# Performance work log

Hardware: AMD Instinct MI355X
Metric: run time of the kernel (lower is better)

## Reference

```python
import jax, jax.numpy as jnp
import numpy as np

EMBED = 1024
HEADS = 16
HEAD_DIM = EMBED // HEADS
BASE = 10000.0


def _rope_cos_sin(seq_len, dim, dtype):
    inv_freq = 1.0 / (BASE ** (jnp.arange(0, dim, 2, dtype=jnp.float32) / dim))
    t = jnp.arange(seq_len, dtype=jnp.float32)
    freqs = jnp.einsum('i,j->ij', t, inv_freq)           # [S, dim/2]
    emb = jnp.concatenate([freqs, freqs], axis=-1)        # [S, dim]
    return jnp.cos(emb).astype(dtype), jnp.sin(emb).astype(dtype)


def _rotate_half(x):
    d = x.shape[-1] // 2
    return jnp.concatenate([-x[..., d:], x[..., :d]], axis=-1)


def setup_inputs() -> dict:
    key = jax.random.key(0)
    ks = jax.random.split(key, 7)
    B, S = 2, 2048
    scale = 0.02
    return {
        'query': jax.random.normal(ks[0], (B, S, EMBED), jnp.float32),
        'key': jax.random.normal(ks[1], (B, S, EMBED), jnp.float32),
        'value': jax.random.normal(ks[2], (B, S, EMBED), jnp.float32),
        'Wq': jax.random.normal(ks[3], (EMBED, EMBED), jnp.float32) * scale,
        'Wk': jax.random.normal(ks[4], (EMBED, EMBED), jnp.float32) * scale,
        'Wv': jax.random.normal(ks[5], (EMBED, EMBED), jnp.float32) * scale,
        'Wo': jax.random.normal(ks[6], (EMBED, EMBED), jnp.float32) * scale,
    }


def reference(query, key, value, Wq, Wk, Wv, Wo):
    B, Sq, _ = query.shape
    Sk = key.shape[1]
    # projections (bias-free Linear: x @ W^T; W sampled so use x @ W directly)
    q = (query @ Wq).reshape(B, Sq, HEADS, HEAD_DIM).transpose(0, 2, 1, 3)  # [B,H,Sq,Dh]
    k = (key @ Wk).reshape(B, Sk, HEADS, HEAD_DIM).transpose(0, 2, 1, 3)
    v = (value @ Wv).reshape(B, Sk, HEADS, HEAD_DIM).transpose(0, 2, 1, 3)
    # RoPE applied to q and k per-position
    cos_q, sin_q = _rope_cos_sin(Sq, HEAD_DIM, q.dtype)  # [Sq,Dh]
    cos_k, sin_k = _rope_cos_sin(Sk, HEAD_DIM, k.dtype)
    q = q * cos_q[None, None] + _rotate_half(q) * sin_q[None, None]
    k = k * cos_k[None, None] + _rotate_half(k) * sin_k[None, None]
    scores = jnp.einsum('bhqd,bhkd->bhqk', q, k) / jnp.sqrt(jnp.asarray(HEAD_DIM, q.dtype))
    probs = jax.nn.softmax(scores, axis=-1)
    out = jnp.einsum('bhqk,bhkd->bhqd', probs, v)
    out = out.transpose(0, 2, 1, 3).reshape(B, Sq, EMBED)
    return out @ Wo
```

## Files before the change

### kernel.cpp

```cpp
#include <hip/hip_runtime.h>
#include <hip/hip_bf16.h>


typedef unsigned short u16;
typedef unsigned int u32;
typedef __attribute__((ext_vector_type(8))) short short8;
typedef __attribute__((ext_vector_type(4))) float f32x4;

#define MFMA16(a, b, c) __builtin_amdgcn_mfma_f32_16x16x32_bf16((a), (b), (c), 0, 0, 0)

typedef __attribute__((address_space(3))) u16 lds_u16;
typedef __attribute__((address_space(1))) const u16 glb_u16;

__device__ __forceinline__ void gload16(const u16* g, u16* l) {
    __builtin_amdgcn_global_load_lds((glb_u16*)g, (lds_u16*)l, 16, 0, 0);
}

__device__ __forceinline__ u16 f2bf(float f) {
    __hip_bfloat16 h = __float2bfloat16(f);
    return *reinterpret_cast<u16*>(&h);
}

__global__ __launch_bounds__(256) void conv_x(const float* __restrict__ q,
                                              const float* __restrict__ k,
                                              const float* __restrict__ v,
                                              u16* __restrict__ X3) {
    int z = blockIdx.y;
    const float* src = (z == 0) ? q : (z == 1) ? k : v;
    int i = (blockIdx.x * 256 + threadIdx.x) * 4;
    float4 f = *reinterpret_cast<const float4*>(src + i);
    ushort4 o;
    o.x = f2bf(f.x); o.y = f2bf(f.y); o.z = f2bf(f.z); o.w = f2bf(f.w);
    *reinterpret_cast<ushort4*>(X3 + (size_t)z * 4194304 + i) = o;
}

__global__ __launch_bounds__(256) void transpose_w(const float* __restrict__ w0,
                                                   const float* __restrict__ w1,
                                                   const float* __restrict__ w2,
                                                   const float* __restrict__ w3,
                                                   u16* __restrict__ WT) {
    __shared__ float t[32][33];
    const float* Ws[4] = {w0, w1, w2, w3};
    const float* W = Ws[blockIdx.z];
    int n0 = blockIdx.x * 32, k0 = blockIdx.y * 32;
    int tx = threadIdx.x, ty = threadIdx.y;
    for (int r = 0; r < 4; r++) {
        int kk = ty + r * 8;
        t[kk][tx] = W[(k0 + kk) * 1024 + n0 + tx];
    }
    __syncthreads();
    u16* out = WT + (size_t)blockIdx.z * 1048576;
    for (int r = 0; r < 4; r++) {
        int nn = ty + r * 8;
        out[(n0 + nn) * 1024 + k0 + tx] = f2bf(t[tx][nn]);
    }
}

__global__ __launch_bounds__(256) void rope_table(float2* __restrict__ tab) {
    int gid = blockIdx.x * 256 + threadIdx.x;
    int s = gid >> 5, d = gid & 31;
    float inv = powf(10000.f, -(float)d / 32.f);
    float fr = (float)s * inv;
    tab[gid] = make_float2(cosf(fr), sinf(fr));
}

__global__ __launch_bounds__(256) void gemm_qkv(const u16* __restrict__ Aall,
                                                const u16* __restrict__ WT,
                                                u16* __restrict__ Qp,
                                                u16* __restrict__ Kp,
                                                u16* __restrict__ Vsd,
                                                const float2* __restrict__ tab) {
    int z = blockIdx.z;
    const u16* A  = Aall + (size_t)z * 4194304;
    const u16* Bt = WT + (size_t)z * 1048576;
    const int K = 1024;
    int m0 = blockIdx.y * 128, n0 = blockIdx.x * 128;
    __shared__ u16 As[128 * 32];
    __shared__ u16 Bs[128 * 32];
    int tid = threadIdx.x;
    int wave = tid >> 6, lane = tid & 63, quad = lane >> 4, l16 = lane & 15;
    int wm = (wave >> 1) * 64, wn = (wave & 1) * 64;
    f32x4 acc[4][4];
    for (int i = 0; i < 4; i++)
        for (int j = 0; j < 4; j++)
            for (int r = 0; r < 4; r++) acc[i][j][r] = 0.f;

    for (int k0 = 0; k0 < K; k0 += 32) {
        __syncthreads();
        for (int c = 0; c < 2; c++) {
            int e = (tid + c * 256) * 8;
            int row = e >> 5, col = e & 31;
            gload16(&A[(size_t)(m0 + row) * K + k0 + col], &As[e]);
            gload16(&Bt[(size_t)(n0 + row) * K + k0 + col], &Bs[e]);
        }
        __syncthreads();
        short8 af[4], bfr[4];
        for (int i = 0; i < 4; i++)
            af[i] = *reinterpret_cast<const short8*>(&As[(wm + i * 16 + l16) * 32 + quad * 8]);
        for (int j = 0; j < 4; j++)
            bfr[j] = *reinterpret_cast<const short8*>(&Bs[(wn + j * 16 + l16) * 32 + quad * 8]);
        for (int i = 0; i < 4; i++)
            for (int j = 0; j < 4; j++)
                acc[i][j] = MFMA16(af[i], bfr[j], acc[i][j]);
    }

    int h = (n0 + wn) >> 6;
    if (z == 2) {
        for (int i = 0; i < 4; i++)
            for (int r = 0; r < 4; r++) {
                int m = m0 + wm + i * 16 + quad * 4 + r;
                int b = m >> 11, s = m & 2047;
                u16* row = Vsd + (((size_t)(b * 16 + h)) * 2048 + s) * 64;
                for (int j = 0; j < 4; j++)
                    row[j * 16 + l16] = f2bf(acc[i][j][r]);
            }
    } else {
        u16* base = (z == 0) ? Qp : Kp;
        float scale = (z == 0) ? 0.125f : 1.f;
        for (int i = 0; i < 4; i++)
            for (int r = 0; r < 4; r++) {
                int m = m0 + wm + i * 16 + quad * 4 + r;
                int b = m >> 11, s = m & 2047;
                u16* row = base + (((size_t)(b * 16 + h)) * 2048 + s) * 64;
                for (int j = 0; j < 2; j++) {
                    int d = j * 16 + l16;
                    float2 cs = tab[s * 32 + d];
                    float x1 = acc[i][j][r] * scale;
                    float x2 = acc[i][j + 2][r] * scale;
                    row[d]      = f2bf(x1 * cs.x - x2 * cs.y);
                    row[d + 32] = f2bf(x2 * cs.x + x1 * cs.y);
                }
            }
    }
}

__global__ __launch_bounds__(256) void gemm_bt_f32(const u16* __restrict__ A,
                                                   const u16* __restrict__ Bt,
                                                   float* __restrict__ C,
                                                   int M, int N, int K) {
    int m0 = blockIdx.y * 128, n0 = blockIdx.x * 128;
    __shared__ u16 As[128 * 32];
    __shared__ u16 Bs[128 * 32];
    int tid = threadIdx.x;
    int wave = tid >> 6, lane = tid & 63, quad = lane >> 4, l16 = lane & 15;
    int wm = (wave >> 1) * 64, wn = (wave & 1) * 64;
    f32x4 acc[4][4];
    for (int i = 0; i < 4; i++)
        for (int j = 0; j < 4; j++)
            for (int r = 0; r < 4; r++) acc[i][j][r] = 0.f;

    for (int k0 = 0; k0 < K; k0 += 32) {
        __syncthreads();
        for (int c = 0; c < 2; c++) {
            int e = (tid + c * 256) * 8;
            int row = e >> 5, col = e & 31;
            gload16(&A[(size_t)(m0 + row) * K + k0 + col], &As[e]);
            gload16(&Bt[(size_t)(n0 + row) * K + k0 + col], &Bs[e]);
        }
        __syncthreads();
        short8 af[4], bfr[4];
        for (int i = 0; i < 4; i++)
            af[i] = *reinterpret_cast<const short8*>(&As[(wm + i * 16 + l16) * 32 + quad * 8]);
        for (int j = 0; j < 4; j++)
            bfr[j] = *reinterpret_cast<const short8*>(&Bs[(wn + j * 16 + l16) * 32 + quad * 8]);
        for (int i = 0; i < 4; i++)
            for (int j = 0; j < 4; j++)
                acc[i][j] = MFMA16(af[i], bfr[j], acc[i][j]);
    }

    for (int i = 0; i < 4; i++)
        for (int r = 0; r < 4; r++) {
            int m = m0 + wm + i * 16 + quad * 4 + r;
            for (int j = 0; j < 4; j++)
                C[(size_t)m * N + n0 + wn + j * 16 + l16] = acc[i][j][r];
        }
}

__global__ __launch_bounds__(256) void v_transpose(const u16* __restrict__ Vsd,
                                                   u16* __restrict__ Vt) {
    __shared__ u16 t[64 * 72];
    int s0 = blockIdx.x * 64, bh = blockIdx.y;
    const u16* src = Vsd + (size_t)bh * 131072;
    int tid = threadIdx.x;
    int srow = tid >> 3, scol = (tid & 7) * 8;
    for (int c = 0; c < 2; c++) {
        int s = srow + c * 32;
        *reinterpret_cast<int4*>(&t[s * 72 + scol]) =
            *reinterpret_cast<const int4*>(&src[(size_t)(s0 + s) * 64 + scol]);
    }
    __syncthreads();
    for (int c = 0; c < 2; c++) {
        int d = srow + c * 32;
        short8 o;
        for (int j = 0; j < 8; j++) o[j] = (short)t[(scol + j) * 72 + d];
        *reinterpret_cast<short8*>(&Vt[(size_t)bh * 131072 + (size_t)d * 2048 + s0 + scol]) = o;
    }
}

__global__ __launch_bounds__(256) void flash_attn(const u16* __restrict__ Qp,
                                                  const u16* __restrict__ Kp,
                                                  const u16* __restrict__ Vt_g,
                                                  u16* __restrict__ attn) {
    int q0 = blockIdx.x * 128, bh = blockIdx.y;
    const u16* Q = Qp + (size_t)bh * 131072;
    const u16* K = Kp + (size_t)bh * 131072;
    const u16* Vt = Vt_g + (size_t)bh * 131072;
    __shared__ u16 Ks[64 * 72];
    __shared__ u16 Vs[64 * 72];
    __shared__ u16 Ps[128 * 72];
    int tid = threadIdx.x, wave = tid >> 6, lane = tid & 63;
    int quad = lane >> 4, l16 = lane & 15;
    int srow = tid >> 3, scol = (tid & 7) * 8;

    short8 qf[2][2];
    for (int g = 0; g < 2; g++)
        for (int kk = 0; kk < 2; kk++)
            qf[g][kk] = *reinterpret_cast<const short8*>(
                &Q[(size_t)(q0 + wave * 32 + g * 16 + l16) * 64 + kk * 32 + quad * 8]);

    float psum[2] = {0.f, 0.f};
    f32x4 Oacc[2][4];
    for (int g = 0; g < 2; g++)
        for (int dt = 0; dt < 4; dt++)
            for (int r = 0; r < 4; r++) Oacc[g][dt][r] = 0.f;

    for (int kv0 = 0; kv0 < 2048; kv0 += 64) {
        __syncthreads();
        for (int c = 0; c < 2; c++) {
            int row = srow + c * 32;
            *reinterpret_cast<int4*>(&Ks[row * 72 + scol]) =
                *reinterpret_cast<const int4*>(&K[(size_t)(kv0 + row) * 64 + scol]);
            *reinterpret_cast<int4*>(&Vs[row * 72 + scol]) =
                *reinterpret_cast<const int4*>(&Vt[(size_t)row * 2048 + kv0 + scol]);
        }
        __syncthreads();

        f32x4 st[2][4];
        for (int g = 0; g < 2; g++)
            for (int nt = 0; nt < 4; nt++)
                for (int r = 0; r < 4; r++) st[g][nt][r] = 0.f;
        for (int kk = 0; kk < 2; kk++)
            for (int nt = 0; nt < 4; nt++) {
                short8 af = *reinterpret_cast<const short8*>(
                    &Ks[(nt * 16 + l16) * 72 + kk * 32 + quad * 8]);
                for (int g = 0; g < 2; g++)
                    st[g][nt] = MFMA16(af, qf[g][kk], st[g][nt]);
            }

        for (int g = 0; g < 2; g++)
            for (int nt = 0; nt < 4; nt++) {
                float p0 = __expf(st[g][nt][0]);
                float p1 = __expf(st[g][nt][1]);
                float p2 = __expf(st[g][nt][2]);
                float p3 = __expf(st[g][nt][3]);
                psum[g] += (p0 + p1) + (p2 + p3);
                uint2 w;
                w.x = (u32)f2bf(p0) | ((u32)f2bf(p1) << 16);
                w.y = (u32)f2bf(p2) | ((u32)f2bf(p3) << 16);
                *reinterpret_cast<uint2*>(
                    &Ps[(wave * 32 + g * 16 + l16) * 72 + nt * 16 + quad * 4]) = w;
            }

        for (int kk = 0; kk < 2; kk++) {
            short8 pa[2];
            for (int g = 0; g < 2; g++)
                pa[g] = *reinterpret_cast<const short8*>(
                    &Ps[(wave * 32 + g * 16 + l16) * 72 + kk * 32 + quad * 8]);
            for (int dt = 0; dt < 4; dt++) {
                short8 bv = *reinterpret_cast<const short8*>(
                    &Vs[(dt * 16 + l16) * 72 + kk * 32 + quad * 8]);
                for (int g = 0; g < 2; g++)
                    Oacc[g][dt] = MFMA16(pa[g], bv, Oacc[g][dt]);
            }
        }
    }

    int b = bh >> 4, h = bh & 15;
    for (int g = 0; g < 2; g++) {
        float ps = psum[g];
        ps += __shfl_xor(ps, 16);
        ps += __shfl_xor(ps, 32);
        float linv[4];
        for (int r = 0; r < 4; r++)
            linv[r] = 1.f / __shfl(ps, quad * 4 + r);
        for (int dt = 0; dt < 4; dt++)
            for (int r = 0; r < 4; r++) {
                int s = q0 + wave * 32 + g * 16 + quad * 4 + r;
                attn[((size_t)(b * 2048 + s)) * 1024 + h * 64 + dt * 16 + l16] =
                    f2bf(Oacc[g][dt][r] * linv[r]);
            }
    }
}

extern "C" void kernel_launch(void* const* d_in, const int* in_sizes, int n_in,
                              void* d_out, int out_size, void* d_ws, size_t ws_size,
                              hipStream_t stream) {
    const float* q  = (const float*)d_in[0];
    const float* k  = (const float*)d_in[1];
    const float* v  = (const float*)d_in[2];
    const float* wq = (const float*)d_in[3];
    const float* wk = (const float*)d_in[4];
    const float* wv = (const float*)d_in[5];
    const float* wo = (const float*)d_in[6];

    u16* ws = (u16*)d_ws;
    u16* WT  = ws;
    u16* X3  = ws + (size_t)4 * 1048576;
    u16* QKV = X3 + (size_t)3 * 4194304;
    u16* Qp  = QKV;
    u16* Kp  = QKV + (size_t)1 * 4194304;
    u16* Vsd = QKV + (size_t)2 * 4194304;
    u16* attn = X3;
    u16* Vt_g = X3 + (size_t)2 * 4194304;
    float2* tab = (float2*)d_out;

    conv_x<<<dim3(4096, 3), 256, 0, stream>>>(q, k, v, X3);
    transpose_w<<<dim3(32, 32, 4), dim3(32, 8), 0, stream>>>(wq, wk, wv, wo, WT);
    rope_table<<<256, 256, 0, stream>>>(tab);
    gemm_qkv<<<dim3(8, 32, 3), 256, 0, stream>>>(X3, WT, Qp, Kp, Vsd, tab);
    v_transpose<<<dim3(32, 32), 256, 0, stream>>>(Vsd, Vt_g);
    flash_attn<<<dim3(16, 32), 256, 0, stream>>>(Qp, Kp, Vt_g, attn);
    gemm_bt_f32<<<dim3(8, 32, 1), 256, 0, stream>>>(
        attn, WT + (size_t)3 * 1048576, (float*)d_out, 4096, 1024, 1024);
}
```

Measured before the change: 275.9 us.

## Split KV tile across wave halves in flash attention with LDS reduction

Restructures the attention kernel to use 512 threads per block over 64 query rows. Each block loads a 128-key tile, and two groups of four waves each process one 64-key half. At the end the partial outputs and row sums are combined through shared memory. Blocks double from 512 to 1024, which is meant to fill more CUs and raise occupancy. In exchange the kernel pays for extra LDS traffic, a final cross-wave reduction with added syncs, and a larger per-block LDS footprint. The code skips max subtraction, which the original version also relied on.

```diff
diff --git a/kernel.cpp b/kernel.cpp
--- a/kernel.cpp
+++ b/kernel.cpp
@@ -197,97 +197,104 @@
     }
 }
 
-__global__ __launch_bounds__(256) void flash_attn(const u16* __restrict__ Qp,
-                                                  const u16* __restrict__ Kp,
-                                                  const u16* __restrict__ Vt_g,
-                                                  u16* __restrict__ attn) {
-    int q0 = blockIdx.x * 128, bh = blockIdx.y;
+__global__ __launch_bounds__(512, 6) void flash_attn(const u16* __restrict__ Qp,
+                                                     const u16* __restrict__ Kp,
+                                                     const u16* __restrict__ Vt_g,
+                                                     u16* __restrict__ attn) {
+    int q0 = blockIdx.x * 64, bh = blockIdx.y;
     const u16* Q = Qp + (size_t)bh * 131072;
     const u16* K = Kp + (size_t)bh * 131072;
     const u16* Vt = Vt_g + (size_t)bh * 131072;
-    __shared__ u16 Ks[64 * 72];
-    __shared__ u16 Vs[64 * 72];
-    __shared__ u16 Ps[128 * 72];
+    __shared__ u16 Ks[128 * 72];
+    __shared__ u16 Vs[64 * 136];
+    __shared__ u16 Ps[64 * 136];
     int tid = threadIdx.x, wave = tid >> 6, lane = tid & 63;
     int quad = lane >> 4, l16 = lane & 15;
-    int srow = tid >> 3, scol = (tid & 7) * 8;
-
-    short8 qf[2][2];
-    for (int g = 0; g < 2; g++)
-        for (int kk = 0; kk < 2; kk++)
-            qf[g][kk] = *reinterpret_cast<const short8*>(
-                &Q[(size_t)(q0 + wave * 32 + g * 16 + l16) * 64 + kk * 32 + quad * 8]);
-
-    float psum[2] = {0.f, 0.f};
-    f32x4 Oacc[2][4];
-    for (int g = 0; g < 2; g++)
-        for (int dt = 0; dt < 4; dt++)
-            for (int r = 0; r < 4; r++) Oacc[g][dt][r] = 0.f;
-
-    for (int kv0 = 0; kv0 < 2048; kv0 += 64) {
+    int qg = wave & 3;
+    int kh = wave >> 2;
+
+    short8 qf[2];
+    for (int kk = 0; kk < 2; kk++)
+        qf[kk] = *reinterpret_cast<const short8*>(
+            &Q[(size_t)(q0 + qg * 16 + l16) * 64 + kk * 32 + quad * 8]);
+
+    float psum = 0.f;
+    f32x4 Oacc[4];
+    for (int dt = 0; dt < 4; dt++)
+        for (int r = 0; r < 4; r++) Oacc[dt][r] = 0.f;
+
+    for (int kv0 = 0; kv0 < 2048; kv0 += 128) {
         __syncthreads();
         for (int c = 0; c < 2; c++) {
-            int row = srow + c * 32;
-            *reinterpret_cast<int4*>(&Ks[row * 72 + scol]) =
-                *reinterpret_cast<const int4*>(&K[(size_t)(kv0 + row) * 64 + scol]);
-            *reinterpret_cast<int4*>(&Vs[row * 72 + scol]) =
-                *reinterpret_cast<const int4*>(&Vt[(size_t)row * 2048 + kv0 + scol]);
-        }
-        __syncthreads();
-
-        f32x4 st[2][4];
-        for (int g = 0; g < 2; g++)
-            for (int nt = 0; nt < 4; nt++)
-                for (int r = 0; r < 4; r++) st[g][nt][r] = 0.f;
+            int idx = tid + c * 512;
+            int krow = idx >> 3, kcol = (idx & 7) * 8;
+            *reinterpret_cast<int4*>(&Ks[krow * 72 + kcol]) =
+                *reinterpret_cast<const int4*>(&K[(size_t)(kv0 + krow) * 64 + kcol]);
+            int vrow = idx >> 4, vcol = (idx & 15) * 8;
+            *reinterpret_cast<int4*>(&Vs[vrow * 136 + vcol]) =
+                *reinterpret_cast<const int4*>(&Vt[(size_t)vrow * 2048 + kv0 + vcol]);
+        }
+        __syncthreads();
+
+        f32x4 st[4];
+        for (int nt = 0; nt < 4; nt++)
+            for (int r = 0; r < 4; r++) st[nt][r] = 0.f;
         for (int kk = 0; kk < 2; kk++)
             for (int nt = 0; nt < 4; nt++) {
                 short8 af = *reinterpret_cast<const short8*>(
-                    &Ks[(nt * 16 + l16) * 72 + kk * 32 + quad * 8]);
-                for (int g = 0; g < 2; g++)
-                    st[g][nt] = MFMA16(af, qf[g][kk], st[g][nt]);
-            }
-
-        for (int g = 0; g < 2; g++)
-            for (int nt = 0; nt < 4; nt++) {
-                float p0 = __expf(st[g][nt][0]);
-                float p1 = __expf(st[g][nt][1]);
-                float p2 = __expf(st[g][nt][2]);
-                float p3 = __expf(st[g][nt][3]);
-                psum[g] += (p0 + p1) + (p2 + p3);
-                uint2 w;
-                w.x = (u32)f2bf(p0) | ((u32)f2bf(p1) << 16);
-                w.y = (u32)f2bf(p2) | ((u32)f2bf(p3) << 16);
-                *reinterpret_cast<uint2*>(
-                    &Ps[(wave * 32 + g * 16 + l16) * 72 + nt * 16 + quad * 4]) = w;
-            }
+                    &Ks[(kh * 64 + nt * 16 + l16) * 72 + kk * 32 + quad * 8]);
+                st[nt] = MFMA16(af, qf[kk], st[nt]);
+            }
+
+        for (int nt = 0; nt < 4; nt++) {
+            float p0 = __expf(st[nt][0]);
+            float p1 = __expf(st[nt][1]);
+            float p2 = __expf(st[nt][2]);
+            float p3 = __expf(st[nt][3]);
+            psum += (p0 + p1) + (p2 + p3);
+            uint2 w;
+            w.x = (u32)f2bf(p0) | ((u32)f2bf(p1) << 16);
+            w.y = (u32)f2bf(p2) | ((u32)f2bf(p3) << 16);
+            *reinterpret_cast<uint2*>(
+                &Ps[(qg * 16 + l16) * 136 + kh * 64 + nt * 16 + quad * 4]) = w;
+        }
 
         for (int kk = 0; kk < 2; kk++) {
-            short8 pa[2];
-            for (int g = 0; g < 2; g++)
-                pa[g] = *reinterpret_cast<const short8*>(
-                    &Ps[(wave * 32 + g * 16 + l16) * 72 + kk * 32 + quad * 8]);
+            short8 pa = *reinterpret_cast<const short8*>(
+                &Ps[(qg * 16 + l16) * 136 + kh * 64 + kk * 32 + quad * 8]);
             for (int dt = 0; dt < 4; dt++) {
                 short8 bv = *reinterpret_cast<const short8*>(
-                    &Vs[(dt * 16 + l16) * 72 + kk * 32 + quad * 8]);
-                for (int g = 0; g < 2; g++)
-                    Oacc[g][dt] = MFMA16(pa[g], bv, Oacc[g][dt]);
-            }
-        }
-    }
-
-    int b = bh >> 4, h = bh & 15;
-    for (int g = 0; g < 2; g++) {
-        float ps = psum[g];
-        ps += __shfl_xor(ps, 16);
-        ps += __shfl_xor(ps, 32);
+                    &Vs[(dt * 16 + l16) * 136 + kh * 64 + kk * 32 + quad * 8]);
+                Oacc[dt] = MFMA16(pa, bv, Oacc[dt]);
+            }
+        }
+    }
+
+    psum += __shfl_xor(psum, 16);
+    psum += __shfl_xor(psum, 32);
+
+    float* Of = reinterpret_cast<float*>(Ks);
+    float* ph = reinterpret_cast<float*>(&Ks[8192]);
+    __syncthreads();
+    if (kh == 1) {
+        for (int dt = 0; dt < 4; dt++)
+            for (int r = 0; r < 4; r++)
+                Of[(qg * 16 + quad * 4 + r) * 64 + dt * 16 + l16] = Oacc[dt][r];
+        if (quad == 0) ph[qg * 16 + l16] = psum;
+    }
+    __syncthreads();
+    if (kh == 0) {
+        psum += ph[qg * 16 + l16];
         float linv[4];
         for (int r = 0; r < 4; r++)
-            linv[r] = 1.f / __shfl(ps, quad * 4 + r);
+            linv[r] = 1.f / __shfl(psum, quad * 4 + r);
+        int b = bh >> 4, h = bh & 15;
         for (int dt = 0; dt < 4; dt++)
             for (int r = 0; r < 4; r++) {
-                int s = q0 + wave * 32 + g * 16 + quad * 4 + r;
+                float o = Oacc[dt][r] + Of[(qg * 16 + quad * 4 + r) * 64 + dt * 16 + l16];
+                int s = q0 + qg * 16 + quad * 4 + r;
                 attn[((size_t)(b * 2048 + s)) * 1024 + h * 64 + dt * 16 + l16] =
-                    f2bf(Oacc[g][dt][r] * linv[r]);
+                    f2bf(o * linv[r]);
             }
     }
 }
@@ -319,7 +326,7 @@
     rope_table<<<256, 256, 0, stream>>>(tab);
     gemm_qkv<<<dim3(8, 32, 3), 256, 0, stream>>>(X3, WT, Qp, Kp, Vsd, tab);
     v_transpose<<<dim3(32, 32), 256, 0, stream>>>(Vsd, Vt_g);
-    flash_attn<<<dim3(16, 32), 256, 0, stream>>>(Qp, Kp, Vt_g, attn);
+    flash_attn<<<dim3(32, 32), 512, 0, stream>>>(Qp, Kp, Vt_g, attn);
     gemm_bt_f32<<<dim3(8, 32, 1), 256, 0, stream>>>(
         attn, WT + (size_t)3 * 1048576, (float*)d_out, 4096, 1024, 1024);
 }
```

Result: no change. 278.7 us (+1.0%).

## Fuse V transpose into QKV GEMM epilogue and split KV across waves in attention

Applied to the files above, without the earlier changes.

The V projection epilogue now writes V directly in the transposed [d, s] layout, which removes the separate v_transpose kernel and its extra round trip through global memory. Flash attention now uses 512 threads per block. Two wave groups each handle half of a 128-key tile, and their partial outputs and row sums are merged through LDS at the end. This doubles the wave-level parallelism and halves the number of loop iterations, at the cost of more LDS, a final reduction step, and less coalesced strided stores in the GEMM epilogue.

```diff
diff --git a/kernel.cpp b/kernel.cpp
--- a/kernel.cpp
+++ b/kernel.cpp
@@ -68,7 +68,7 @@
                                                 const u16* __restrict__ WT,
                                                 u16* __restrict__ Qp,
                                                 u16* __restrict__ Kp,
-                                                u16* __restrict__ Vsd,
+                                                u16* __restrict__ Vt,
                                                 const float2* __restrict__ tab) {
     int z = blockIdx.z;
     const u16* A  = Aall + (size_t)z * 4194304;
@@ -106,14 +106,20 @@
 
     int h = (n0 + wn) >> 6;
     if (z == 2) {
-        for (int i = 0; i < 4; i++)
-            for (int r = 0; r < 4; r++) {
-                int m = m0 + wm + i * 16 + quad * 4 + r;
-                int b = m >> 11, s = m & 2047;
-                u16* row = Vsd + (((size_t)(b * 16 + h)) * 2048 + s) * 64;
-                for (int j = 0; j < 4; j++)
-                    row[j * 16 + l16] = f2bf(acc[i][j][r]);
-            }
+        for (int i = 0; i < 4; i++) {
+            int mbase = m0 + wm + i * 16 + quad * 4;
+            int b = mbase >> 11, sb = mbase & 2047;
+            for (int j = 0; j < 4; j++) {
+                int d = j * 16 + l16;
+                ushort4 o;
+                o.x = f2bf(acc[i][j][0]);
+                o.y = f2bf(acc[i][j][1]);
+                o.z = f2bf(acc[i][j][2]);
+                o.w = f2bf(acc[i][j][3]);
+                *reinterpret_cast<ushort4*>(
+                    &Vt[((size_t)(b * 16 + h)) * 131072 + (size_t)d * 2048 + sb]) = o;
+            }
+        }
     } else {
         u16* base = (z == 0) ? Qp : Kp;
         float scale = (z == 0) ? 0.125f : 1.f;
@@ -176,47 +182,28 @@
         }
 }
 
-__global__ __launch_bounds__(256) void v_transpose(const u16* __restrict__ Vsd,
-                                                   u16* __restrict__ Vt) {
-    __shared__ u16 t[64 * 72];
-    int s0 = blockIdx.x * 64, bh = blockIdx.y;
-    const u16* src = Vsd + (size_t)bh * 131072;
-    int tid = threadIdx.x;
-    int srow = tid >> 3, scol = (tid & 7) * 8;
-    for (int c = 0; c < 2; c++) {
-        int s = srow + c * 32;
-        *reinterpret_cast<int4*>(&t[s * 72 + scol]) =
-            *reinterpret_cast<const int4*>(&src[(size_t)(s0 + s) * 64 + scol]);
-    }
-    __syncthreads();
-    for (int c = 0; c < 2; c++) {
-        int d = srow + c * 32;
-        short8 o;
-        for (int j = 0; j < 8; j++) o[j] = (short)t[(scol + j) * 72 + d];
-        *reinterpret_cast<short8*>(&Vt[(size_t)bh * 131072 + (size_t)d * 2048 + s0 + scol]) = o;
-    }
-}
-
-__global__ __launch_bounds__(256) void flash_attn(const u16* __restrict__ Qp,
-                                                  const u16* __restrict__ Kp,
-                                                  const u16* __restrict__ Vt_g,
-                                                  u16* __restrict__ attn) {
+__global__ __launch_bounds__(512, 4) void flash_attn(const u16* __restrict__ Qp,
+                                                     const u16* __restrict__ Kp,
+                                                     const u16* __restrict__ Vt_g,
+                                                     u16* __restrict__ attn) {
     int q0 = blockIdx.x * 128, bh = blockIdx.y;
     const u16* Q = Qp + (size_t)bh * 131072;
     const u16* K = Kp + (size_t)bh * 131072;
     const u16* Vt = Vt_g + (size_t)bh * 131072;
-    __shared__ u16 Ks[64 * 72];
-    __shared__ u16 Vs[64 * 72];
-    __shared__ u16 Ps[128 * 72];
+    __shared__ u16 smem[35328];
+    u16* Ks = smem;
+    u16* Vs = smem + 9216;
+    u16* Ps = smem + 17920;
     int tid = threadIdx.x, wave = tid >> 6, lane = tid & 63;
     int quad = lane >> 4, l16 = lane & 15;
-    int srow = tid >> 3, scol = (tid & 7) * 8;
+    int qg = wave & 3;
+    int kh = wave >> 2;
 
     short8 qf[2][2];
     for (int g = 0; g < 2; g++)
         for (int kk = 0; kk < 2; kk++)
             qf[g][kk] = *reinterpret_cast<const short8*>(
-                &Q[(size_t)(q0 + wave * 32 + g * 16 + l16) * 64 + kk * 32 + quad * 8]);
+                &Q[(size_t)(q0 + qg * 32 + g * 16 + l16) * 64 + kk * 32 + quad * 8]);
 
     float psum[2] = {0.f, 0.f};
     f32x4 Oacc[2][4];
@@ -224,14 +211,16 @@
         for (int dt = 0; dt < 4; dt++)
             for (int r = 0; r < 4; r++) Oacc[g][dt][r] = 0.f;
 
-    for (int kv0 = 0; kv0 < 2048; kv0 += 64) {
+    for (int kv0 = 0; kv0 < 2048; kv0 += 128) {
         __syncthreads();
         for (int c = 0; c < 2; c++) {
-            int row = srow + c * 32;
-            *reinterpret_cast<int4*>(&Ks[row * 72 + scol]) =
-                *reinterpret_cast<const int4*>(&K[(size_t)(kv0 + row) * 64 + scol]);
-            *reinterpret_cast<int4*>(&Vs[row * 72 + scol]) =
-                *reinterpret_cast<const int4*>(&Vt[(size_t)row * 2048 + kv0 + scol]);
+            int idx = tid + c * 512;
+            int krow = idx >> 3, kcol = (idx & 7) * 8;
+            *reinterpret_cast<int4*>(&Ks[krow * 72 + kcol]) =
+                *reinterpret_cast<const int4*>(&K[(size_t)(kv0 + krow) * 64 + kcol]);
+            int vrow = idx >> 4, vcol = (idx & 15) * 8;
+            *reinterpret_cast<int4*>(&Vs[vrow * 136 + vcol]) =
+                *reinterpret_cast<const int4*>(&Vt[(size_t)vrow * 2048 + kv0 + vcol]);
         }
         __syncthreads();
 
@@ -242,7 +231,7 @@
         for (int kk = 0; kk < 2; kk++)
             for (int nt = 0; nt < 4; nt++) {
                 short8 af = *reinterpret_cast<const short8*>(
-                    &Ks[(nt * 16 + l16) * 72 + kk * 32 + quad * 8]);
+                    &Ks[(kh * 64 + nt * 16 + l16) * 72 + kk * 32 + quad * 8]);
                 for (int g = 0; g < 2; g++)
                     st[g][nt] = MFMA16(af, qf[g][kk], st[g][nt]);
             }
@@ -258,37 +247,56 @@
                 w.x = (u32)f2bf(p0) | ((u32)f2bf(p1) << 16);
                 w.y = (u32)f2bf(p2) | ((u32)f2bf(p3) << 16);
                 *reinterpret_cast<uint2*>(
-                    &Ps[(wave * 32 + g * 16 + l16) * 72 + nt * 16 + quad * 4]) = w;
+                    &Ps[(qg * 32 + g * 16 + l16) * 136 + kh * 64 + nt * 16 + quad * 4]) = w;
             }
 
         for (int kk = 0; kk < 2; kk++) {
             short8 pa[2];
             for (int g = 0; g < 2; g++)
                 pa[g] = *reinterpret_cast<const short8*>(
-                    &Ps[(wave * 32 + g * 16 + l16) * 72 + kk * 32 + quad * 8]);
+                    &Ps[(qg * 32 + g * 16 + l16) * 136 + kh * 64 + kk * 32 + quad * 8]);
             for (int dt = 0; dt < 4; dt++) {
                 short8 bv = *reinterpret_cast<const short8*>(
-                    &Vs[(dt * 16 + l16) * 72 + kk * 32 + quad * 8]);
+                    &Vs[(dt * 16 + l16) * 136 + kh * 64 + kk * 32 + quad * 8]);
                 for (int g = 0; g < 2; g++)
                     Oacc[g][dt] = MFMA16(pa[g], bv, Oacc[g][dt]);
             }
         }
     }
 
-    int b = bh >> 4, h = bh & 15;
     for (int g = 0; g < 2; g++) {
-        float ps = psum[g];
-        ps += __shfl_xor(ps, 16);
-        ps += __shfl_xor(ps, 32);
-        float linv[4];
-        for (int r = 0; r < 4; r++)
-            linv[r] = 1.f / __shfl(ps, quad * 4 + r);
-        for (int dt = 0; dt < 4; dt++)
-            for (int r = 0; r < 4; r++) {
-                int s = q0 + wave * 32 + g * 16 + quad * 4 + r;
-                attn[((size_t)(b * 2048 + s)) * 1024 + h * 64 + dt * 16 + l16] =
-                    f2bf(Oacc[g][dt][r] * linv[r]);
-            }
+        psum[g] += __shfl_xor(psum[g], 16);
+        psum[g] += __shfl_xor(psum[g], 32);
+    }
+
+    float* Of = reinterpret_cast<float*>(smem);
+    float* ph = Of + 128 * 65;
+    __syncthreads();
+    if (kh == 1) {
+        for (int g = 0; g < 2; g++) {
+            for (int dt = 0; dt < 4; dt++)
+                for (int r = 0; r < 4; r++)
+                    Of[(qg * 32 + g * 16 + quad * 4 + r) * 65 + dt * 16 + l16] = Oacc[g][dt][r];
+            if (quad == 0) ph[qg * 32 + g * 16 + l16] = psum[g];
+        }
+    }
+    __syncthreads();
+    if (kh == 0) {
+        int b = bh >> 4, h = bh & 15;
+        for (int g = 0; g < 2; g++) {
+            float ps = psum[g] + ph[qg * 32 + g * 16 + l16];
+            float linv[4];
+            for (int r = 0; r < 4; r++)
+                linv[r] = 1.f / __shfl(ps, quad * 4 + r);
+            for (int dt = 0; dt < 4; dt++)
+                for (int r = 0; r < 4; r++) {
+                    float o = Oacc[g][dt][r] +
+                              Of[(qg * 32 + g * 16 + quad * 4 + r) * 65 + dt * 16 + l16];
+                    int s = q0 + qg * 32 + g * 16 + quad * 4 + r;
+                    attn[((size_t)(b * 2048 + s)) * 1024 + h * 64 + dt * 16 + l16] =
+                        f2bf(o * linv[r]);
+                }
+        }
     }
 }
 
@@ -309,17 +317,15 @@
     u16* QKV = X3 + (size_t)3 * 4194304;
     u16* Qp  = QKV;
     u16* Kp  = QKV + (size_t)1 * 4194304;
-    u16* Vsd = QKV + (size_t)2 * 4194304;
+    u16* Vt_g = QKV + (size_t)2 * 4194304;
     u16* attn = X3;
-    u16* Vt_g = X3 + (size_t)2 * 4194304;
     float2* tab = (float2*)d_out;
 
     conv_x<<<dim3(4096, 3), 256, 0, stream>>>(q, k, v, X3);
     transpose_w<<<dim3(32, 32, 4), dim3(32, 8), 0, stream>>>(wq, wk, wv, wo, WT);
     rope_table<<<256, 256, 0, stream>>>(tab);
-    gemm_qkv<<<dim3(8, 32, 3), 256, 0, stream>>>(X3, WT, Qp, Kp, Vsd, tab);
-    v_transpose<<<dim3(32, 32), 256, 0, stream>>>(Vsd, Vt_g);
-    flash_attn<<<dim3(16, 32), 256, 0, stream>>>(Qp, Kp, Vt_g, attn);
+    gemm_qkv<<<dim3(8, 32, 3), 256, 0, stream>>>(X3, WT, Qp, Kp, Vt_g, tab);
+    flash_attn<<<dim3(16, 32), 512, 0, stream>>>(Qp, Kp, Vt_g, attn);
     gemm_bt_f32<<<dim3(8, 32, 1), 256, 0, stream>>>(
         attn, WT + (size_t)3 * 1048576, (float*)d_out, 4096, 1024, 1024);
 }
```

New measurement: 250.0 us. 1.1x faster.
